# Optimization experiments

Hardware: AMD Instinct MI355X
Metric: run time of the kernel (lower is better)

## Reference

```python
import jax, jax.numpy as jnp
import numpy as np

D_MODEL = 1024
N_HEADS = 16
D_K = D_MODEL // N_HEADS


def setup_inputs() -> dict:
    key = jax.random.key(0)
    ks = jax.random.split(key, 9)
    s = 1.0 / np.sqrt(D_MODEL)
    inp = {
        "x": jax.random.normal(ks[0], (4, 2048, D_MODEL), dtype=jnp.float32),
        "wq": jax.random.normal(ks[1], (D_MODEL, D_MODEL), dtype=jnp.float32) * s,
        "bq": jax.random.normal(ks[2], (D_MODEL,), dtype=jnp.float32) * 0.01,
        "wk": jax.random.normal(ks[3], (D_MODEL, D_MODEL), dtype=jnp.float32) * s,
        "bk": jax.random.normal(ks[4], (D_MODEL,), dtype=jnp.float32) * 0.01,
        "wv": jax.random.normal(ks[5], (D_MODEL, D_MODEL), dtype=jnp.float32) * s,
        "bv": jax.random.normal(ks[6], (D_MODEL,), dtype=jnp.float32) * 0.01,
        "wo": jax.random.normal(ks[7], (D_MODEL, D_MODEL), dtype=jnp.float32) * s,
        "bo": jax.random.normal(ks[8], (D_MODEL,), dtype=jnp.float32) * 0.01,
    }
    return inp


def reference(x, wq, bq, wk, bk, wv, bv, wo, bo):
    B, S, _ = x.shape
    # QKV projections (weights stored [in, out] so y = x @ w + b)
    q = (x @ wq + bq).reshape(B, S, N_HEADS, D_K).transpose(0, 2, 1, 3)  # [B,H,S,Dk]
    k = (x @ wk + bk).reshape(B, S, N_HEADS, D_K).transpose(0, 2, 1, 3)
    v = (x @ wv + bv).reshape(B, S, N_HEADS, D_K).transpose(0, 2, 1, 3)
    scale = 1.0 / jnp.sqrt(jnp.asarray(D_K, dtype=x.dtype))
    scores = jnp.einsum("bhqd,bhkd->bhqk", q, k) * scale  # [B,H,S,S]
    attn = jax.nn.softmax(scores, axis=-1)
    out = jnp.einsum("bhqk,bhkd->bhqd", attn, v)  # [B,H,S,Dk]
    out = out.transpose(0, 2, 1, 3).reshape(B, S, D_MODEL)
    return out @ wo + bo
```

## Files before the change

kernel.cpp:

```cpp
#include <hip/hip_runtime.h>

#define D_MODEL 1024
#define NH 16
#define DK 64
#define BB 4
#define SS 2048
#define MROWS (BB*SS)

typedef __attribute__((ext_vector_type(4))) float f32x4;
typedef __attribute__((ext_vector_type(16))) float f32x16;
typedef __attribute__((ext_vector_type(8))) short short8;
typedef __attribute__((ext_vector_type(4))) float float4v;
typedef __attribute__((ext_vector_type(2))) unsigned u32x2;

typedef const __attribute__((address_space(1))) void* gas_t;
typedef __attribute__((address_space(3))) void* las_t;

static __device__ __forceinline__ ushort f2bf(float f) {
  union { float f; unsigned u; } v; v.f = f;
  unsigned r = 0x7fffu + ((v.u >> 16) & 1u);
  return (ushort)((v.u + r) >> 16);
}

__global__ __launch_bounds__(256) void convert_x_k(const float* __restrict__ x,
                                                   ushort* __restrict__ xb) {
  int i = blockIdx.x * 256 + threadIdx.x;
  float4v v = ((const float4v*)x)[i];
  ushort4 o;
  o.x = f2bf(v.x); o.y = f2bf(v.y); o.z = f2bf(v.z); o.w = f2bf(v.w);
  ((ushort4*)xb)[i] = o;
}

__global__ __launch_bounds__(256) void convert_wt_k(const float* __restrict__ w,
                                                    ushort* __restrict__ wt) {
  __shared__ float tile[64][65];
  int bx = blockIdx.x, by = blockIdx.y;
  int tx = threadIdx.x & 63, ty = threadIdx.x >> 6;
#pragma unroll
  for (int i = 0; i < 16; ++i) {
    int r = i * 4 + ty;
    tile[r][tx] = w[(size_t)(by * 64 + r) * D_MODEL + bx * 64 + tx];
  }
  __syncthreads();
#pragma unroll
  for (int i = 0; i < 16; ++i) {
    int r = i * 4 + ty;
    wt[(size_t)(bx * 64 + r) * D_MODEL + by * 64 + tx] = f2bf(tile[tx][r]);
  }
}

__global__ __launch_bounds__(256) void gemm_qkv_k(const ushort* __restrict__ A,
                                                  const ushort* __restrict__ Bt,
                                                  const float* __restrict__ bq,
                                                  const float* __restrict__ bk,
                                                  const float* __restrict__ bv,
                                                  ushort* __restrict__ Qw,
                                                  ushort* __restrict__ Kw,
                                                  ushort* __restrict__ Vw,
                                                  float qscale) {
  const int K = D_MODEL;
  __shared__ __align__(16) ushort As[128 * 32];
  __shared__ __align__(16) ushort Bs[128 * 32];
  const int nbn = 24;
  int bid = blockIdx.x;
  int wg = (bid & 7) * 192 + (bid >> 3);
  int bm = wg / nbn, bn = wg % nbn;
  const int t = threadIdx.x;
  const int l = t & 63;
  const int w = t >> 6;
  const int g = l >> 4, q = l & 15;
  const int wr = w >> 1, wc = w & 1;

  f32x4 acc[4][4];
#pragma unroll
  for (int m = 0; m < 4; ++m)
#pragma unroll
    for (int n = 0; n < 4; ++n) acc[m][n] = f32x4{0.f, 0.f, 0.f, 0.f};

  const ushort* Ab = A + (size_t)bm * 128 * K;
  const ushort* Bb = Bt + (size_t)bn * 128 * K;

  for (int kt = 0; kt < K; kt += 32) {
    __syncthreads();
#pragma unroll
    for (int i = 0; i < 2; ++i) {
      int c = i * 256 + t;
      __builtin_amdgcn_global_load_lds((gas_t)(Ab + (size_t)(c >> 2) * K + kt + (c & 3) * 8),
                                       (las_t)(As + c * 8), 16, 0, 0);
      __builtin_amdgcn_global_load_lds((gas_t)(Bb + (size_t)(c >> 2) * K + kt + (c & 3) * 8),
                                       (las_t)(Bs + c * 8), 16, 0, 0);
    }
    __syncthreads();
    short8 af[4], bf[4];
#pragma unroll
    for (int m = 0; m < 4; ++m)
      af[m] = *(const short8*)(As + (wr * 64 + m * 16 + q) * 32 + g * 8);
#pragma unroll
    for (int n = 0; n < 4; ++n)
      bf[n] = *(const short8*)(Bs + (wc * 64 + n * 16 + q) * 32 + g * 8);
#pragma unroll
    for (int m = 0; m < 4; ++m)
#pragma unroll
      for (int n = 0; n < 4; ++n)
        acc[m][n] = __builtin_amdgcn_mfma_f32_16x16x32_bf16(af[m], bf[n], acc[m][n], 0, 0, 0);
  }

  const int sec = (bn * 128) >> 10;
  const float* bias = sec == 0 ? bq : (sec == 1 ? bk : bv);
  const float scale = sec == 0 ? qscale : 1.0f;
  ushort* dst = sec == 0 ? Qw : Kw;
  const int rbase0 = bm * 128 + wr * 64 + g * 4;
  const int cbase = (bn * 128 + wc * 64 + q) & 1023;
#pragma unroll
  for (int m = 0; m < 4; ++m) {
    int r0 = rbase0 + m * 16;
#pragma unroll
    for (int n = 0; n < 4; ++n) {
      int c = cbase + n * 16;
      float bv_ = bias[c];
      if (sec == 2) {
        ushort4 pk;
        pk.x = f2bf(acc[m][n][0] + bv_);
        pk.y = f2bf(acc[m][n][1] + bv_);
        pk.z = f2bf(acc[m][n][2] + bv_);
        pk.w = f2bf(acc[m][n][3] + bv_);
        size_t off = (((size_t)((r0 >> 11) * NH + (c >> 6))) * DK + (c & 63)) * (size_t)SS + (r0 & (SS - 1));
        *(ushort4*)(Vw + off) = pk;
      } else {
#pragma unroll
        for (int j = 0; j < 4; ++j) {
          int r = r0 + j;
          float v = (acc[m][n][j] + bv_) * scale;
          size_t off = (((size_t)((r >> 11) * NH + (c >> 6))) * SS + (r & (SS - 1))) * DK + (c & 63);
          dst[off] = f2bf(v);
        }
      }
    }
  }
}

__global__ __launch_bounds__(256) void gemm_out_k(const ushort* __restrict__ A,
                                                  const ushort* __restrict__ Bt,
                                                  const float* __restrict__ bias,
                                                  float* __restrict__ outp) {
  const int K = D_MODEL;
  __shared__ __align__(16) ushort As[128 * 32];
  __shared__ __align__(16) ushort Bs[128 * 32];
  const int nbn = 8;
  int bid = blockIdx.x;
  int wg = (bid & 7) * 64 + (bid >> 3);
  int bm = wg / nbn, bn = wg % nbn;
  const int t = threadIdx.x;
  const int l = t & 63;
  const int w = t >> 6;
  const int g = l >> 4, q = l & 15;
  const int wr = w >> 1, wc = w & 1;

  f32x4 acc[4][4];
#pragma unroll
  for (int m = 0; m < 4; ++m)
#pragma unroll
    for (int n = 0; n < 4; ++n) acc[m][n] = f32x4{0.f, 0.f, 0.f, 0.f};

  const ushort* Ab = A + (size_t)bm * 128 * K;
  const ushort* Bb = Bt + (size_t)bn * 128 * K;

  for (int kt = 0; kt < K; kt += 32) {
    __syncthreads();
#pragma unroll
    for (int i = 0; i < 2; ++i) {
      int c = i * 256 + t;
      __builtin_amdgcn_global_load_lds((gas_t)(Ab + (size_t)(c >> 2) * K + kt + (c & 3) * 8),
                                       (las_t)(As + c * 8), 16, 0, 0);
      __builtin_amdgcn_global_load_lds((gas_t)(Bb + (size_t)(c >> 2) * K + kt + (c & 3) * 8),
                                       (las_t)(Bs + c * 8), 16, 0, 0);
    }
    __syncthreads();
    short8 af[4], bf[4];
#pragma unroll
    for (int m = 0; m < 4; ++m)
      af[m] = *(const short8*)(As + (wr * 64 + m * 16 + q) * 32 + g * 8);
#pragma unroll
    for (int n = 0; n < 4; ++n)
      bf[n] = *(const short8*)(Bs + (wc * 64 + n * 16 + q) * 32 + g * 8);
#pragma unroll
    for (int m = 0; m < 4; ++m)
#pragma unroll
      for (int n = 0; n < 4; ++n)
        acc[m][n] = __builtin_amdgcn_mfma_f32_16x16x32_bf16(af[m], bf[n], acc[m][n], 0, 0, 0);
  }

  const int rbase0 = bm * 128 + wr * 64 + g * 4;
  const int cbase = bn * 128 + wc * 64 + q;
#pragma unroll
  for (int m = 0; m < 4; ++m) {
    int r0 = rbase0 + m * 16;
#pragma unroll
    for (int n = 0; n < 4; ++n) {
      int c = cbase + n * 16;
      float bv = bias[c];
#pragma unroll
      for (int j = 0; j < 4; ++j)
        outp[(size_t)(r0 + j) * D_MODEL + c] = acc[m][n][j] + bv;
    }
  }
}

__global__ __launch_bounds__(256, 2) void attn_k(const ushort* __restrict__ Qm,
                                                 const ushort* __restrict__ Km,
                                                 const ushort* __restrict__ Vm,
                                                 ushort* __restrict__ Ob) {
  __shared__ __align__(16) ushort Ks[2][64 * 64];
  __shared__ __align__(16) ushort Vs[2][64 * 64];
  const int bid = blockIdx.x;
  const int logical = (bid & 7) * 64 + (bid >> 3);
  const int bh = logical >> 3;
  const int qblk = logical & 7;
  const int t = threadIdx.x, l = t & 63, w = t >> 6;
  const int q = l & 31, h = l >> 5;
  const int qsw = q & 7;

  const ushort* Qb = Qm + ((size_t)bh * SS + qblk * 256 + w * 64) * DK;
  const ushort* Kb = Km + (size_t)bh * SS * DK;
  const ushort* Vb = Vm + (size_t)bh * DK * SS;

  short8 qf[2][4];
#pragma unroll
  for (int qg = 0; qg < 2; ++qg)
#pragma unroll
    for (int ks = 0; ks < 4; ++ks)
      qf[qg][ks] = *(const short8*)(Qb + (qg * 32 + q) * DK + ks * 16 + h * 8);

  f32x16 zf;
#pragma unroll
  for (int r = 0; r < 16; ++r) zf[r] = 0.f;

  f32x16 oacc[2][2];
#pragma unroll
  for (int qg = 0; qg < 2; ++qg)
#pragma unroll
    for (int d = 0; d < 2; ++d) oacc[qg][d] = zf;
  float lrun[2] = {0.f, 0.f};

  const int cg = (l & 7) ^ ((l >> 3) & 7);

#define STAGE(B, KT)                                                                        \
  do {                                                                                      \
    _Pragma("unroll") for (int i_ = 0; i_ < 2; ++i_) {                                      \
      int row_ = w * 16 + i_ * 8 + (l >> 3);                                                \
      __builtin_amdgcn_global_load_lds((gas_t)(Kb + (size_t)((KT) + row_) * DK + cg * 8),   \
                                       (las_t)(Ks[B] + (w * 16 + i_ * 8) * 64 + l * 8),     \
                                       16, 0, 0);                                           \
      __builtin_amdgcn_global_load_lds((gas_t)(Vb + (size_t)row_ * SS + (KT) + cg * 8),     \
                                       (las_t)(Vs[B] + (w * 16 + i_ * 8) * 64 + l * 8),     \
                                       16, 0, 0);                                           \
    }                                                                                       \
  } while (0)

#define SOFTMAX_PACK(QG, SC, PF)                                                            \
  do {                                                                                      \
    _Pragma("unroll") for (int n = 0; n < 2; ++n)                                           \
      _Pragma("unroll") for (int r = 0; r < 16; ++r)                                        \
        SC[n][r] = __builtin_amdgcn_exp2f(SC[n][r]);                                        \
    float s8[8];                                                                            \
    _Pragma("unroll") for (int i = 0; i < 8; ++i)                                           \
      s8[i] = (SC[0][i] + SC[0][i + 8]) + (SC[1][i] + SC[1][i + 8]);                        \
    _Pragma("unroll") for (int i = 0; i < 4; ++i) s8[i] += s8[i + 4];                       \
    lrun[QG] += (s8[0] + s8[1]) + (s8[2] + s8[3]);                                          \
    _Pragma("unroll") for (int n = 0; n < 2; ++n) {                                         \
      unsigned wv[8];                                                                       \
      _Pragma("unroll") for (int Qd = 0; Qd < 4; ++Qd) {                                    \
        unsigned w0, w1;                                                                    \
        asm("v_cvt_pk_bf16_f32 %0, %1, %2" : "=v"(w0)                                       \
            : "v"(SC[n][Qd * 4 + 0]), "v"(SC[n][Qd * 4 + 1]));                              \
        asm("v_cvt_pk_bf16_f32 %0, %1, %2" : "=v"(w1)                                       \
            : "v"(SC[n][Qd * 4 + 2]), "v"(SC[n][Qd * 4 + 3]));                              \
        wv[Qd * 2] = w0; wv[Qd * 2 + 1] = w1;                                               \
      }                                                                                     \
      _Pragma("unroll") for (int m = 0; m < 2; ++m) {                                       \
        u32x2 r0 = __builtin_amdgcn_permlane32_swap(wv[(2 * m) * 2 + 0],                    \
                                                    wv[(2 * m + 1) * 2 + 0], false, false); \
        u32x2 r1 = __builtin_amdgcn_permlane32_swap(wv[(2 * m) * 2 + 1],                    \
                                                    wv[(2 * m + 1) * 2 + 1], false, false); \
        union { unsigned u[4]; short8 s; } fu;                                              \
        fu.u[0] = r0[0]; fu.u[1] = r1[0]; fu.u[2] = r0[1]; fu.u[3] = r1[1];                 \
        PF[n * 2 + m] = fu.s;                                                               \
      }                                                                                     \
    }                                                                                       \
  } while (0)

  STAGE(0, 0);
  int cur = 0;

  for (int kt = 0; kt < SS; kt += 64) {
    __syncthreads();
    if (kt + 64 < SS) STAGE(cur ^ 1, kt + 64);

    const ushort* Kc = Ks[cur];
    const ushort* Vc = Vs[cur];

    short8 kf[2][4];
#pragma unroll
    for (int ks = 0; ks < 4; ++ks) {
      int ch = ((ks * 2 + h) ^ qsw) * 8;
#pragma unroll
      for (int n = 0; n < 2; ++n)
        kf[n][ks] = *(const short8*)(Kc + (n * 32 + q) * 64 + ch);
    }

    f32x16 sc0[2], sc1[2];
    __builtin_amdgcn_s_setprio(1);
#pragma unroll
    for (int n = 0; n < 2; ++n)
      sc0[n] = __builtin_amdgcn_mfma_f32_32x32x16_bf16(kf[n][0], qf[0][0], zf, 0, 0, 0);
#pragma unroll
    for (int ks = 1; ks < 4; ++ks)
#pragma unroll
      for (int n = 0; n < 2; ++n)
        sc0[n] = __builtin_amdgcn_mfma_f32_32x32x16_bf16(kf[n][ks], qf[0][ks], sc0[n], 0, 0, 0);
#pragma unroll
    for (int n = 0; n < 2; ++n)
      sc1[n] = __builtin_amdgcn_mfma_f32_32x32x16_bf16(kf[n][0], qf[1][0], zf, 0, 0, 0);
#pragma unroll
    for (int ks = 1; ks < 4; ++ks)
#pragma unroll
      for (int n = 0; n < 2; ++n)
        sc1[n] = __builtin_amdgcn_mfma_f32_32x32x16_bf16(kf[n][ks], qf[1][ks], sc1[n], 0, 0, 0);
    __builtin_amdgcn_s_setprio(0);

    short8 vf[2][4];
#pragma unroll
    for (int kvb = 0; kvb < 4; ++kvb) {
      int ch = ((kvb * 2 + h) ^ qsw) * 8;
#pragma unroll
      for (int d = 0; d < 2; ++d)
        vf[d][kvb] = *(const short8*)(Vc + (d * 32 + q) * 64 + ch);
    }

    short8 pf0[4], pf1[4];
    SOFTMAX_PACK(0, sc0, pf0);
    __builtin_amdgcn_s_setprio(1);
#pragma unroll
    for (int kvb = 0; kvb < 4; ++kvb)
#pragma unroll
      for (int d = 0; d < 2; ++d)
        oacc[0][d] = __builtin_amdgcn_mfma_f32_32x32x16_bf16(vf[d][kvb], pf0[kvb], oacc[0][d], 0, 0, 0);
    __builtin_amdgcn_s_setprio(0);

    SOFTMAX_PACK(1, sc1, pf1);
    __builtin_amdgcn_s_setprio(1);
#pragma unroll
    for (int kvb = 0; kvb < 4; ++kvb)
#pragma unroll
      for (int d = 0; d < 2; ++d)
        oacc[1][d] = __builtin_amdgcn_mfma_f32_32x32x16_bf16(vf[d][kvb], pf1[kvb], oacc[1][d], 0, 0, 0);
    __builtin_amdgcn_s_setprio(0);
    cur ^= 1;
  }
#undef STAGE
#undef SOFTMAX_PACK

  const int b_ = bh >> 4, h_ = bh & 15;
#pragma unroll
  for (int qg = 0; qg < 2; ++qg) {
    float lt = lrun[qg];
    lt += __shfl_xor(lt, 32);
    float inv = 1.0f / lt;
    const int srow = qblk * 256 + w * 64 + qg * 32 + q;
#pragma unroll
    for (int d = 0; d < 2; ++d)
#pragma unroll
      for (int rq = 0; rq < 4; ++rq) {
        ushort4 pk;
        pk.x = f2bf(oacc[qg][d][rq * 4 + 0] * inv);
        pk.y = f2bf(oacc[qg][d][rq * 4 + 1] * inv);
        pk.z = f2bf(oacc[qg][d][rq * 4 + 2] * inv);
        pk.w = f2bf(oacc[qg][d][rq * 4 + 3] * inv);
        size_t off = ((size_t)b_ * SS + srow) * D_MODEL + h_ * 64 + d * 32 + rq * 8 + h * 4;
        *(ushort4*)(Ob + off) = pk;
      }
  }
}

extern "C" void kernel_launch(void* const* d_in, const int* in_sizes, int n_in,
                              void* d_out, int out_size, void* d_ws, size_t ws_size,
                              hipStream_t stream) {
  (void)in_sizes; (void)n_in; (void)out_size; (void)ws_size;
  const float* x  = (const float*)d_in[0];
  const float* wq = (const float*)d_in[1];
  const float* bq = (const float*)d_in[2];
  const float* wk = (const float*)d_in[3];
  const float* bk = (const float*)d_in[4];
  const float* wv = (const float*)d_in[5];
  const float* bv = (const float*)d_in[6];
  const float* wo = (const float*)d_in[7];
  const float* bo = (const float*)d_in[8];

  char* ws = (char*)d_ws;
  ushort* xb    = (ushort*)(ws);
  ushort* wqkvt = (ushort*)(ws + 16777216);
  ushort* wot   = (ushort*)(ws + 16777216 + 6291456);
  ushort* Qw    = (ushort*)(ws + 16777216 + 6291456 + 2097152);
  ushort* Kw    = (ushort*)(ws + 16777216 + 6291456 + 2097152 + 16777216);
  ushort* Vw    = (ushort*)(ws + 16777216 + 6291456 + 2097152 + 2 * 16777216);
  ushort* Obw   = xb;

  convert_x_k<<<MROWS * D_MODEL / 4 / 256, 256, 0, stream>>>(x, xb);
  convert_wt_k<<<dim3(16, 16), 256, 0, stream>>>(wq, wqkvt);
  convert_wt_k<<<dim3(16, 16), 256, 0, stream>>>(wk, wqkvt + 1024 * 1024);
  convert_wt_k<<<dim3(16, 16), 256, 0, stream>>>(wv, wqkvt + 2 * 1024 * 1024);
  convert_wt_k<<<dim3(16, 16), 256, 0, stream>>>(wo, wot);

  gemm_qkv_k<<<1536, 256, 0, stream>>>(xb, wqkvt, bq, bk, bv, Qw, Kw, Vw,
                                       0.125f * 1.44269504088896f);

  attn_k<<<512, 256, 0, stream>>>(Qw, Kw, Vw, Obw);

  gemm_out_k<<<512, 256, 0, stream>>>(Obw, wot, bo, (float*)d_out);
}
```

Before: 201.8 us.

## Halve per-wave query rows in attention to raise occupancy

Each wave in the attention kernel now handles 32 query rows instead of 64. The block count doubles to 1024 and launch bounds rise to 4 blocks per CU. This cuts register pressure (one set of score and output accumulators) so more waves can hide latency. The cost is that every K/V tile staged in LDS is reused by half as many query rows, which doubles total K/V global and LDS traffic.

```diff
diff --git a/kernel.cpp b/kernel.cpp
--- a/kernel.cpp
+++ b/kernel.cpp
@@ -206,41 +206,35 @@
   }
 }
 
-__global__ __launch_bounds__(256, 2) void attn_k(const ushort* __restrict__ Qm,
+__global__ __launch_bounds__(256, 4) void attn_k(const ushort* __restrict__ Qm,
                                                  const ushort* __restrict__ Km,
                                                  const ushort* __restrict__ Vm,
                                                  ushort* __restrict__ Ob) {
   __shared__ __align__(16) ushort Ks[2][64 * 64];
   __shared__ __align__(16) ushort Vs[2][64 * 64];
   const int bid = blockIdx.x;
-  const int logical = (bid & 7) * 64 + (bid >> 3);
-  const int bh = logical >> 3;
-  const int qblk = logical & 7;
+  const int logical = (bid & 7) * 128 + (bid >> 3);
+  const int bh = logical >> 4;
+  const int qblk = logical & 15;
   const int t = threadIdx.x, l = t & 63, w = t >> 6;
   const int q = l & 31, h = l >> 5;
   const int qsw = q & 7;
 
-  const ushort* Qb = Qm + ((size_t)bh * SS + qblk * 256 + w * 64) * DK;
+  const ushort* Qb = Qm + ((size_t)bh * SS + qblk * 128 + w * 32) * DK;
   const ushort* Kb = Km + (size_t)bh * SS * DK;
   const ushort* Vb = Vm + (size_t)bh * DK * SS;
 
-  short8 qf[2][4];
-#pragma unroll
-  for (int qg = 0; qg < 2; ++qg)
-#pragma unroll
-    for (int ks = 0; ks < 4; ++ks)
-      qf[qg][ks] = *(const short8*)(Qb + (qg * 32 + q) * DK + ks * 16 + h * 8);
-
-  f32x16 zf;
-#pragma unroll
-  for (int r = 0; r < 16; ++r) zf[r] = 0.f;
-
-  f32x16 oacc[2][2];
-#pragma unroll
-  for (int qg = 0; qg < 2; ++qg)
-#pragma unroll
-    for (int d = 0; d < 2; ++d) oacc[qg][d] = zf;
-  float lrun[2] = {0.f, 0.f};
+  short8 qf[4];
+#pragma unroll
+  for (int ks = 0; ks < 4; ++ks)
+    qf[ks] = *(const short8*)(Qb + q * DK + ks * 16 + h * 8);
+
+  f32x16 oacc[2];
+#pragma unroll
+  for (int d = 0; d < 2; ++d)
+#pragma unroll
+    for (int r = 0; r < 16; ++r) oacc[d][r] = 0.f;
+  float lrun = 0.f;
 
   const int cg = (l & 7) ^ ((l >> 3) & 7);
 
@@ -257,38 +251,6 @@
     }                                                                                       \
   } while (0)
 
-#define SOFTMAX_PACK(QG, SC, PF)                                                            \
-  do {                                                                                      \
-    _Pragma("unroll") for (int n = 0; n < 2; ++n)                                           \
-      _Pragma("unroll") for (int r = 0; r < 16; ++r)                                        \
-        SC[n][r] = __builtin_amdgcn_exp2f(SC[n][r]);                                        \
-    float s8[8];                                                                            \
-    _Pragma("unroll") for (int i = 0; i < 8; ++i)                                           \
-      s8[i] = (SC[0][i] + SC[0][i + 8]) + (SC[1][i] + SC[1][i + 8]);                        \
-    _Pragma("unroll") for (int i = 0; i < 4; ++i) s8[i] += s8[i + 4];                       \
-    lrun[QG] += (s8[0] + s8[1]) + (s8[2] + s8[3]);                                          \
-    _Pragma("unroll") for (int n = 0; n < 2; ++n) {                                         \
-      unsigned wv[8];                                                                       \
-      _Pragma("unroll") for (int Qd = 0; Qd < 4; ++Qd) {                                    \
-        unsigned w0, w1;                                                                    \
-        asm("v_cvt_pk_bf16_f32 %0, %1, %2" : "=v"(w0)                                       \
-            : "v"(SC[n][Qd * 4 + 0]), "v"(SC[n][Qd * 4 + 1]));                              \
-        asm("v_cvt_pk_bf16_f32 %0, %1, %2" : "=v"(w1)                                       \
-            : "v"(SC[n][Qd * 4 + 2]), "v"(SC[n][Qd * 4 + 3]));                              \
-        wv[Qd * 2] = w0; wv[Qd * 2 + 1] = w1;                                               \
-      }                                                                                     \
-      _Pragma("unroll") for (int m = 0; m < 2; ++m) {                                       \
-        u32x2 r0 = __builtin_amdgcn_permlane32_swap(wv[(2 * m) * 2 + 0],                    \
-                                                    wv[(2 * m + 1) * 2 + 0], false, false); \
-        u32x2 r1 = __builtin_amdgcn_permlane32_swap(wv[(2 * m) * 2 + 1],                    \
-                                                    wv[(2 * m + 1) * 2 + 1], false, false); \
-        union { unsigned u[4]; short8 s; } fu;                                              \
-        fu.u[0] = r0[0]; fu.u[1] = r1[0]; fu.u[2] = r0[1]; fu.u[3] = r1[1];                 \
-        PF[n * 2 + m] = fu.s;                                                               \
-      }                                                                                     \
-    }                                                                                       \
-  } while (0)
-
   STAGE(0, 0);
   int cur = 0;
 
@@ -299,87 +261,88 @@
     const ushort* Kc = Ks[cur];
     const ushort* Vc = Vs[cur];
 
-    short8 kf[2][4];
+    f32x16 sc[2];
+#pragma unroll
+    for (int n = 0; n < 2; ++n)
+#pragma unroll
+      for (int r = 0; r < 16; ++r) sc[n][r] = 0.f;
+
+    __builtin_amdgcn_s_setprio(1);
 #pragma unroll
     for (int ks = 0; ks < 4; ++ks) {
       int ch = ((ks * 2 + h) ^ qsw) * 8;
-#pragma unroll
-      for (int n = 0; n < 2; ++n)
-        kf[n][ks] = *(const short8*)(Kc + (n * 32 + q) * 64 + ch);
-    }
-
-    f32x16 sc0[2], sc1[2];
+      short8 kf0 = *(const short8*)(Kc + q * 64 + ch);
+      short8 kf1 = *(const short8*)(Kc + (32 + q) * 64 + ch);
+      sc[0] = __builtin_amdgcn_mfma_f32_32x32x16_bf16(kf0, qf[ks], sc[0], 0, 0, 0);
+      sc[1] = __builtin_amdgcn_mfma_f32_32x32x16_bf16(kf1, qf[ks], sc[1], 0, 0, 0);
+    }
+    __builtin_amdgcn_s_setprio(0);
+
+#pragma unroll
+    for (int n = 0; n < 2; ++n)
+#pragma unroll
+      for (int r = 0; r < 16; ++r) sc[n][r] = __builtin_amdgcn_exp2f(sc[n][r]);
+
+    float s8[8];
+#pragma unroll
+    for (int i = 0; i < 8; ++i)
+      s8[i] = (sc[0][i] + sc[0][i + 8]) + (sc[1][i] + sc[1][i + 8]);
+#pragma unroll
+    for (int i = 0; i < 4; ++i) s8[i] += s8[i + 4];
+    lrun += (s8[0] + s8[1]) + (s8[2] + s8[3]);
+
+    short8 pf[4];
+#pragma unroll
+    for (int n = 0; n < 2; ++n) {
+      unsigned wv[8];
+#pragma unroll
+      for (int Qd = 0; Qd < 4; ++Qd) {
+        unsigned w0, w1;
+        asm("v_cvt_pk_bf16_f32 %0, %1, %2" : "=v"(w0) : "v"(sc[n][Qd * 4 + 0]), "v"(sc[n][Qd * 4 + 1]));
+        asm("v_cvt_pk_bf16_f32 %0, %1, %2" : "=v"(w1) : "v"(sc[n][Qd * 4 + 2]), "v"(sc[n][Qd * 4 + 3]));
+        wv[Qd * 2] = w0; wv[Qd * 2 + 1] = w1;
+      }
+#pragma unroll
+      for (int m = 0; m < 2; ++m) {
+        u32x2 r0 = __builtin_amdgcn_permlane32_swap(wv[(2 * m) * 2 + 0], wv[(2 * m + 1) * 2 + 0], false, false);
+        u32x2 r1 = __builtin_amdgcn_permlane32_swap(wv[(2 * m) * 2 + 1], wv[(2 * m + 1) * 2 + 1], false, false);
+        union { unsigned u[4]; short8 s; } fu;
+        fu.u[0] = r0[0]; fu.u[1] = r1[0]; fu.u[2] = r0[1]; fu.u[3] = r1[1];
+        pf[n * 2 + m] = fu.s;
+      }
+    }
+
     __builtin_amdgcn_s_setprio(1);
-#pragma unroll
-    for (int n = 0; n < 2; ++n)
-      sc0[n] = __builtin_amdgcn_mfma_f32_32x32x16_bf16(kf[n][0], qf[0][0], zf, 0, 0, 0);
-#pragma unroll
-    for (int ks = 1; ks < 4; ++ks)
-#pragma unroll
-      for (int n = 0; n < 2; ++n)
-        sc0[n] = __builtin_amdgcn_mfma_f32_32x32x16_bf16(kf[n][ks], qf[0][ks], sc0[n], 0, 0, 0);
-#pragma unroll
-    for (int n = 0; n < 2; ++n)
-      sc1[n] = __builtin_amdgcn_mfma_f32_32x32x16_bf16(kf[n][0], qf[1][0], zf, 0, 0, 0);
-#pragma unroll
-    for (int ks = 1; ks < 4; ++ks)
-#pragma unroll
-      for (int n = 0; n < 2; ++n)
-        sc1[n] = __builtin_amdgcn_mfma_f32_32x32x16_bf16(kf[n][ks], qf[1][ks], sc1[n], 0, 0, 0);
-    __builtin_amdgcn_s_setprio(0);
-
-    short8 vf[2][4];
 #pragma unroll
     for (int kvb = 0; kvb < 4; ++kvb) {
       int ch = ((kvb * 2 + h) ^ qsw) * 8;
-#pragma unroll
-      for (int d = 0; d < 2; ++d)
-        vf[d][kvb] = *(const short8*)(Vc + (d * 32 + q) * 64 + ch);
-    }
-
-    short8 pf0[4], pf1[4];
-    SOFTMAX_PACK(0, sc0, pf0);
-    __builtin_amdgcn_s_setprio(1);
-#pragma unroll
-    for (int kvb = 0; kvb < 4; ++kvb)
-#pragma unroll
-      for (int d = 0; d < 2; ++d)
-        oacc[0][d] = __builtin_amdgcn_mfma_f32_32x32x16_bf16(vf[d][kvb], pf0[kvb], oacc[0][d], 0, 0, 0);
-    __builtin_amdgcn_s_setprio(0);
-
-    SOFTMAX_PACK(1, sc1, pf1);
-    __builtin_amdgcn_s_setprio(1);
-#pragma unroll
-    for (int kvb = 0; kvb < 4; ++kvb)
-#pragma unroll
-      for (int d = 0; d < 2; ++d)
-        oacc[1][d] = __builtin_amdgcn_mfma_f32_32x32x16_bf16(vf[d][kvb], pf1[kvb], oacc[1][d], 0, 0, 0);
+      short8 vf0 = *(const short8*)(Vc + q * 64 + ch);
+      short8 vf1 = *(const short8*)(Vc + (32 + q) * 64 + ch);
+      oacc[0] = __builtin_amdgcn_mfma_f32_32x32x16_bf16(vf0, pf[kvb], oacc[0], 0, 0, 0);
+      oacc[1] = __builtin_amdgcn_mfma_f32_32x32x16_bf16(vf1, pf[kvb], oacc[1], 0, 0, 0);
+    }
     __builtin_amdgcn_s_setprio(0);
     cur ^= 1;
   }
 #undef STAGE
-#undef SOFTMAX_PACK
 
   const int b_ = bh >> 4, h_ = bh & 15;
-#pragma unroll
-  for (int qg = 0; qg < 2; ++qg) {
-    float lt = lrun[qg];
-    lt += __shfl_xor(lt, 32);
-    float inv = 1.0f / lt;
-    const int srow = qblk * 256 + w * 64 + qg * 32 + q;
-#pragma unroll
-    for (int d = 0; d < 2; ++d)
-#pragma unroll
-      for (int rq = 0; rq < 4; ++rq) {
-        ushort4 pk;
-        pk.x = f2bf(oacc[qg][d][rq * 4 + 0] * inv);
-        pk.y = f2bf(oacc[qg][d][rq * 4 + 1] * inv);
-        pk.z = f2bf(oacc[qg][d][rq * 4 + 2] * inv);
-        pk.w = f2bf(oacc[qg][d][rq * 4 + 3] * inv);
-        size_t off = ((size_t)b_ * SS + srow) * D_MODEL + h_ * 64 + d * 32 + rq * 8 + h * 4;
-        *(ushort4*)(Ob + off) = pk;
-      }
-  }
+  float lt = lrun;
+  lt += __shfl_xor(lt, 32);
+  float inv = 1.0f / lt;
+  const int srow = qblk * 128 + w * 32 + q;
+#pragma unroll
+  for (int d = 0; d < 2; ++d)
+#pragma unroll
+    for (int rq = 0; rq < 4; ++rq) {
+      ushort4 pk;
+      pk.x = f2bf(oacc[d][rq * 4 + 0] * inv);
+      pk.y = f2bf(oacc[d][rq * 4 + 1] * inv);
+      pk.z = f2bf(oacc[d][rq * 4 + 2] * inv);
+      pk.w = f2bf(oacc[d][rq * 4 + 3] * inv);
+      size_t off = ((size_t)b_ * SS + srow) * D_MODEL + h_ * 64 + d * 32 + rq * 8 + h * 4;
+      *(ushort4*)(Ob + off) = pk;
+    }
 }
 
 extern "C" void kernel_launch(void* const* d_in, const int* in_sizes, int n_in,
@@ -414,7 +377,7 @@
   gemm_qkv_k<<<1536, 256, 0, stream>>>(xb, wqkvt, bq, bk, bv, Qw, Kw, Vw,
                                        0.125f * 1.44269504088896f);
 
-  attn_k<<<512, 256, 0, stream>>>(Qw, Kw, Vw, Obw);
+  attn_k<<<1024, 256, 0, stream>>>(Qw, Kw, Vw, Obw);
 
   gemm_out_k<<<512, 256, 0, stream>>>(Obw, wot, bo, (float*)d_out);
 }
```

Measured after the change: 202.0 us. About the same (+0.1%).
